# Performance work log

Measured on AMD Instinct MI355X. Metric: run time of the kernel, lower is better.

## Reference

```python
import jax, jax.numpy as jnp
import numpy as np

MAX_REL = 16  # block_size//2 = 32//2

def _rel_buckets(T):
    r = jnp.arange(T)
    rel = r[None, :] - r[:, None]              # [T,T] = j - i
    return jnp.clip(rel, -MAX_REL, MAX_REL) + MAX_REL  # [T,T] in [0, 2*MAX_REL]

def setup_inputs() -> dict:
    key = jax.random.key(0)
    ks = jax.random.split(key, 6)
    B, T, C, H = 16, 1024, 64, 64
    x = jax.random.normal(ks[0], (B, T, C), dtype=jnp.float32)
    mask = jnp.tril(jnp.ones((T, T), dtype=jnp.int32))
    Wq = jax.random.normal(ks[1], (C, H), dtype=jnp.float32) * 0.1
    Wk = jax.random.normal(ks[2], (C, H), dtype=jnp.float32) * 0.1
    Wv = jax.random.normal(ks[3], (C, H), dtype=jnp.float32) * 0.1
    rel_key_emb = jax.random.normal(ks[4], (2 * MAX_REL + 1, H), dtype=jnp.float32) * 0.1
    rel_value_emb = jax.random.normal(ks[5], (2 * MAX_REL + 1, H), dtype=jnp.float32) * 0.1
    return {"x": x, "mask": mask, "Wq": Wq, "Wk": Wk, "Wv": Wv,
            "rel_key_emb": rel_key_emb, "rel_value_emb": rel_value_emb}

def reference(x, mask, Wq, Wk, Wv, rel_key_emb, rel_value_emb):
    B, T, C = x.shape
    H = Wq.shape[1]
    scale = H ** -0.5
    q = x @ Wq  # [B,T,H]
    k = x @ Wk
    v = x @ Wv
    buckets = _rel_buckets(T)                 # [T,T] int
    rel_k = rel_key_emb[buckets]              # [T,T,H]
    rel_v = rel_value_emb[buckets]            # [T,T,H]
    content_scores = jnp.einsum('bth,bsh->bts', q, k) * scale     # [B,T,T]
    position_scores = jnp.einsum('bth,tsh->bts', q, rel_k) * scale
    scores = content_scores + position_scores
    scores = jnp.where(mask[None, :, :] == 0, -jnp.inf, scores)
    wei = jax.nn.softmax(scores, axis=-1)     # [B,T,T]  (dropout is identity in eval)
    content_out = jnp.einsum('bts,bsh->bth', wei, v)
    position_out = jnp.einsum('bts,tsh->bth', wei, rel_v)
    return (content_out + position_out, wei)
```

## Files before the change

kernel.cpp:

```cpp
#include <hip/hip_runtime.h>
#include <cstdint>
#include <cstddef>

typedef unsigned short u16;
typedef __attribute__((ext_vector_type(8))) short s16x8;
typedef __attribute__((ext_vector_type(4))) float f32x4;

#define MFMA16(a, b, c) __builtin_amdgcn_mfma_f32_16x16x32_bf16(a, b, c, 0, 0, 0)

#define B_ 16
#define T_ 1024
#define H_ 64
#define SCALE 0.125f

static __device__ __forceinline__ u16 f2bf(float f) {
    unsigned u = __float_as_uint(f);
    u += 0x7FFFu + ((u >> 16) & 1u);
    return (u16)(u >> 16);
}
static __device__ __forceinline__ float bf2f(u16 h) {
    return __uint_as_float((unsigned)h << 16);
}
static __device__ __forceinline__ s16x8 ld8(const u16* p) {
    return *(const s16x8*)p;
}
static __device__ __forceinline__ s16x8 pack8f(const float* p) {
    s16x8 r;
#pragma unroll
    for (int i = 0; i < 8; i++) r[i] = (short)f2bf(p[i]);
    return r;
}

__global__ __launch_bounds__(256) void proj_kernel(
    const float* __restrict__ x, const float* __restrict__ Wq,
    const float* __restrict__ Wk, const float* __restrict__ Wv,
    u16* __restrict__ Qb, u16* __restrict__ Kb, u16* __restrict__ VTb) {
    __shared__ u16 wtb[64][72];
    const int tid = threadIdx.x;
    const int m = blockIdx.y;
    const float* Wm = (m == 0) ? Wq : (m == 1) ? Wk : Wv;
    for (int idx = tid; idx < 1024; idx += 256) {
        const int cin = idx >> 4, c = (idx & 15) << 2;
        const float4 v = *(const float4*)(Wm + cin * 64 + c);
        wtb[c + 0][cin] = f2bf(v.x);
        wtb[c + 1][cin] = f2bf(v.y);
        wtb[c + 2][cin] = f2bf(v.z);
        wtb[c + 3][cin] = f2bf(v.w);
    }
    __syncthreads();
    const int w = tid >> 6, l = tid & 63, lg = l >> 4, lc = l & 15;
    const int base = blockIdx.x * 64 + w * 16;
    const float* xp = x + (size_t)(base + lc) * 64 + lg * 8;
    const s16x8 aX0 = pack8f(xp), aX1 = pack8f(xp + 32);
#pragma unroll
    for (int nt = 0; nt < 4; nt++) {
        const s16x8 b0 = ld8(&wtb[nt * 16 + lc][lg * 8]);
        const s16x8 b1 = ld8(&wtb[nt * 16 + lc][32 + lg * 8]);
        f32x4 acc = {0.f, 0.f, 0.f, 0.f};
        acc = MFMA16(aX0, b0, acc);
        acc = MFMA16(aX1, b1, acc);
        const int col = nt * 16 + lc;
        if (m == 2) {
            const int t0 = base + lg * 4;
            const int bb = t0 >> 10, tl = t0 & 1023;
            ushort4 pk;
            pk.x = f2bf(acc[0]); pk.y = f2bf(acc[1]);
            pk.z = f2bf(acc[2]); pk.w = f2bf(acc[3]);
            *(ushort4*)(VTb + ((size_t)(bb * 64 + col)) * 1024 + tl) = pk;
        } else {
            u16* dst = (m == 0) ? Qb : Kb;
#pragma unroll
            for (int reg = 0; reg < 4; reg++)
                dst[(size_t)(base + lg * 4 + reg) * 64 + col] = f2bf(acc[reg]);
        }
    }
}

__global__ __launch_bounds__(256) void attn_kernel(
    const u16* __restrict__ Qb, const u16* __restrict__ Kb,
    const u16* __restrict__ VTb, const float* __restrict__ rel_key_emb,
    const float* __restrict__ rel_value_emb,
    float* __restrict__ out, float* __restrict__ wei) {
    union EU {
        u16 e[16 * 1024];
        float obuf[4][16][64];
    };
    __shared__ __align__(16) EU sh;
    __shared__ __align__(16) float rv_lds[17][64];
    __shared__ float p_lds[16][33];
    __shared__ float band_lds[16][17];
    __shared__ float sum_lds[4][16];

    const int tid = threadIdx.x, w = tid >> 6, l = tid & 63, lg = l >> 4, lc = l & 15;
    const int bx = blockIdx.x;
    const int s = bx >> 8, i = bx & 255, q = i >> 4;
    const int b = i & 15;
    const int R = (s == 0) ? 63 - q : (s == 1) ? 32 + q : (s == 2) ? 31 - q : q;
    const int wrow = R << 4;
    const int ntiles = R + 1;
    char* eb = (char*)sh.e;

    for (int idx = tid; idx < 17 * 64; idx += 256)
        rv_lds[idx >> 6][idx & 63] = rel_value_emb[idx];
    for (int idx = tid; idx < 16 * 17; idx += 256)
        ((float*)band_lds)[idx] = 0.f;

    const u16* qp = Qb + (size_t)(b * 1024 + wrow + lc) * 64 + lg * 8;
    const s16x8 aQ0 = ld8(qp), aQ1 = ld8(qp + 32);

    if (w == 0) {
#pragma unroll
        for (int nt = 0; nt < 2; nt++) {
            const float* rp = rel_key_emb + (nt * 16 + lc) * 64 + lg * 8;
            const s16x8 b0 = pack8f(rp), b1 = pack8f(rp + 32);
            f32x4 acc = {0.f, 0.f, 0.f, 0.f};
            acc = MFMA16(aQ0, b0, acc);
            acc = MFMA16(aQ1, b1, acc);
#pragma unroll
            for (int reg = 0; reg < 4; reg++)
                p_lds[lg * 4 + reg][nt * 16 + lc] = acc[reg] * SCALE;
        }
    }
    __syncthreads();

    float p0r[4];
#pragma unroll
    for (int reg = 0; reg < 4; reg++) p0r[reg] = p_lds[lg * 4 + reg][0];

    const int P = (ntiles + 1) >> 1;
    const int pq = P >> 2, prem = P & 3;
    const int pstart = w * pq + (w < prem ? w : prem);
    const int pcnt = pq + (w < prem ? 1 : 0);
    const int cbeg = pstart << 1;
    const int cend0 = cbeg + (pcnt << 1);
    const int cend = cend0 < ntiles ? cend0 : ntiles;

    float sum[4] = {0.f, 0.f, 0.f, 0.f};
    f32x4 accO[4];
#pragma unroll
    for (int nt = 0; nt < 4; nt++) accO[nt] = (f32x4){0.f, 0.f, 0.f, 0.f};

    for (int j = 0; j < pcnt; j++) {
        const int sc0 = cbeg + 2 * j;
#pragma unroll
        for (int half = 0; half < 2; half++) {
            const int sc = sc0 + half;
            const int colb = (sc * 16 + lc) * 2;
            if (sc < cend) {
                const u16* kp = Kb + (size_t)(b * 1024 + sc * 16 + lc) * 64 + lg * 8;
                const s16x8 b0 = ld8(kp), b1 = ld8(kp + 32);
                f32x4 acc = {0.f, 0.f, 0.f, 0.f};
                acc = MFMA16(aQ0, b0, acc);
                acc = MFMA16(aQ1, b1, acc);
                const bool bandt = (sc >= ntiles - 2);
#pragma unroll
                for (int reg = 0; reg < 4; reg++) {
                    const int t16 = lg * 4 + reg;
                    const int d = (sc * 16 + lc) - (wrow + t16);
                    float pv = p0r[reg];
                    bool msk = false;
                    if (bandt) {
                        if (d > 0) msk = true;
                        else if (d > -16) pv = p_lds[t16][d + 16];
                    }
                    const float ev = msk ? 0.f : __expf(acc[reg] * SCALE + pv);
                    sum[reg] += ev;
                    *(u16*)(eb + t16 * 2048 + (colb ^ ((t16 & 7) << 4))) = f2bf(ev);
                    if (bandt && d > -16 && d <= 0) band_lds[t16][d + 15] = ev;
                }
            } else {
#pragma unroll
                for (int reg = 0; reg < 4; reg++) {
                    const int t16 = lg * 4 + reg;
                    *(u16*)(eb + t16 * 2048 + (colb ^ ((t16 & 7) << 4))) = 0;
                }
            }
        }
        const int pcolb = sc0 * 32;
        const s16x8 aW =
            *(const s16x8*)(eb + lc * 2048 + ((pcolb + lg * 16) ^ ((lc & 7) << 4)));
#pragma unroll
        for (int nt = 0; nt < 4; nt++) {
            const s16x8 bV =
                ld8(VTb + (size_t)(b * 64 + nt * 16 + lc) * 1024 + sc0 * 16 + lg * 8);
            accO[nt] = MFMA16(aW, bV, accO[nt]);
        }
    }
#pragma unroll
    for (int reg = 0; reg < 4; reg++) {
        sum[reg] += __shfl_xor(sum[reg], 1);
        sum[reg] += __shfl_xor(sum[reg], 2);
        sum[reg] += __shfl_xor(sum[reg], 4);
        sum[reg] += __shfl_xor(sum[reg], 8);
    }
    if (lc == 0) {
#pragma unroll
        for (int reg = 0; reg < 4; reg++) sum_lds[w][lg * 4 + reg] = sum[reg];
    }
    __syncthreads();

    float inv[4];
#pragma unroll
    for (int reg = 0; reg < 4; reg++) {
        const int r = lg * 4 + reg;
        inv[reg] =
            1.0f / (sum_lds[0][r] + sum_lds[1][r] + sum_lds[2][r] + sum_lds[3][r]);
    }
#pragma unroll
    for (int nt = 0; nt < 4; nt++)
#pragma unroll
        for (int reg = 0; reg < 4; reg++) accO[nt][reg] *= inv[reg];

    {
        const int r = tid >> 4;
        const float invr =
            1.0f / (sum_lds[0][r] + sum_lds[1][r] + sum_lds[2][r] + sum_lds[3][r]);
        const int climit = ntiles << 4;
        const int xr = (r & 7) << 4;
        float* wp = wei + ((size_t)b << 20) + (size_t)(wrow + r) * 1024;
        for (int c = (tid & 15) << 2; c < 1024; c += 64) {
            float4 v;
            if (c < climit) {
                const ushort4 ev = *(const ushort4*)(eb + r * 2048 + ((c * 2) ^ xr));
                v.x = bf2f(ev.x) * invr;
                v.y = bf2f(ev.y) * invr;
                v.z = bf2f(ev.z) * invr;
                v.w = bf2f(ev.w) * invr;
            } else {
                v = make_float4(0.f, 0.f, 0.f, 0.f);
            }
            *(float4*)(wp + c) = v;
        }
    }
    __syncthreads();

#pragma unroll
    for (int nt = 0; nt < 4; nt++)
#pragma unroll
        for (int reg = 0; reg < 4; reg++)
            sh.obuf[w][lg * 4 + reg][nt * 16 + lc] = accO[nt][reg];
    __syncthreads();

    {
        const int r = tid >> 4, h = (tid & 15) << 2;
        const float invr =
            1.0f / (sum_lds[0][r] + sum_lds[1][r] + sum_lds[2][r] + sum_lds[3][r]);
        const float4 o0 = *(const float4*)&sh.obuf[0][r][h];
        const float4 o1 = *(const float4*)&sh.obuf[1][r][h];
        const float4 o2 = *(const float4*)&sh.obuf[2][r][h];
        const float4 o3 = *(const float4*)&sh.obuf[3][r][h];
        float a0 = o0.x + o1.x + o2.x + o3.x;
        float a1 = o0.y + o1.y + o2.y + o3.y;
        float a2 = o0.z + o1.z + o2.z + o3.z;
        float a3 = o0.w + o1.w + o2.w + o3.w;
        float bsum = 0.f;
#pragma unroll
        for (int k = 0; k < 16; k++) bsum += band_lds[r][k];
        const float w0 = 1.f - invr * bsum;
        const float4 rv0 = *(const float4*)&rv_lds[0][h];
        a0 += w0 * rv0.x; a1 += w0 * rv0.y; a2 += w0 * rv0.z; a3 += w0 * rv0.w;
#pragma unroll
        for (int k = 0; k < 16; k++) {
            const float bw = band_lds[r][k] * invr;
            const float4 rvk = *(const float4*)&rv_lds[k + 1][h];
            a0 += bw * rvk.x; a1 += bw * rvk.y; a2 += bw * rvk.z; a3 += bw * rvk.w;
        }
        float4 ov; ov.x = a0; ov.y = a1; ov.z = a2; ov.w = a3;
        *(float4*)(out + (size_t)(b * 1024 + wrow + r) * 64 + h) = ov;
    }
}

extern "C" void kernel_launch(void* const* d_in, const int* in_sizes, int n_in,
                              void* d_out, int out_size, void* d_ws, size_t ws_size,
                              hipStream_t stream) {
    const float* x = (const float*)d_in[0];
    const float* Wq = (const float*)d_in[2];
    const float* Wk = (const float*)d_in[3];
    const float* Wv = (const float*)d_in[4];
    const float* rk = (const float*)d_in[5];
    const float* rvv = (const float*)d_in[6];

    float* out = (float*)d_out;
    float* wei = out + (size_t)B_ * T_ * H_;

    u16* Qb = (u16*)d_ws;
    u16* Kb = Qb + (size_t)B_ * T_ * H_;
    u16* VTb = Kb + (size_t)B_ * T_ * H_;

    proj_kernel<<<dim3(256, 3), 256, 0, stream>>>(x, Wq, Wk, Wv, Qb, Kb, VTb);
    attn_kernel<<<dim3(1024), 256, 0, stream>>>(Qb, Kb, VTb, rk, rvv, out, wei);
}
```

Measured before the change: 39.96 us.

## Split attention-weight output into separate recompute kernel using stored row normalizers

The attention kernel no longer keeps the full 16x1024 bf16 probability row block in LDS or writes the 64 MB wei matrix. It stores only per-row inverse sums, and its LDS scratch shrinks to a small per-wave 16x32 tile. A new third kernel recomputes QK^T plus the positional bias and exp, scales by the stored inverse, and writes wei with nontemporal stores. The aim is higher occupancy and more streaming-friendly writes in the attention kernel, paid for with recomputed scores and an extra launch. Recomputing in fp32 from the bf16 score rather than from the bf16-rounded exp may also shift wei values slightly.

Result: slower. 53.81 us (+34.7%).

```diff
diff --git a/kernel.cpp b/kernel.cpp
--- a/kernel.cpp
+++ b/kernel.cpp
@@ -18,9 +18,6 @@
     u += 0x7FFFu + ((u >> 16) & 1u);
     return (u16)(u >> 16);
 }
-static __device__ __forceinline__ float bf2f(u16 h) {
-    return __uint_as_float((unsigned)h << 16);
-}
 static __device__ __forceinline__ s16x8 ld8(const u16* p) {
     return *(const s16x8*)p;
 }
@@ -29,6 +26,11 @@
 #pragma unroll
     for (int i = 0; i < 8; i++) r[i] = (short)f2bf(p[i]);
     return r;
+}
+static __device__ __forceinline__ void slotmap(int bx, int& R, int& b) {
+    const int s = bx >> 8, i = bx & 255, q = i >> 4;
+    b = i & 15;
+    R = (s == 0) ? 63 - q : (s == 1) ? 32 + q : (s == 2) ? 31 - q : q;
 }
 
 __global__ __launch_bounds__(256) void proj_kernel(
@@ -80,25 +82,22 @@
     const u16* __restrict__ Qb, const u16* __restrict__ Kb,
     const u16* __restrict__ VTb, const float* __restrict__ rel_key_emb,
     const float* __restrict__ rel_value_emb,
-    float* __restrict__ out, float* __restrict__ wei) {
-    union EU {
-        u16 e[16 * 1024];
+    float* __restrict__ out, float* __restrict__ invArr) {
+    union SU {
+        u16 w_lds[4][16][40];
         float obuf[4][16][64];
     };
-    __shared__ __align__(16) EU sh;
+    __shared__ __align__(16) SU sh;
     __shared__ __align__(16) float rv_lds[17][64];
     __shared__ float p_lds[16][33];
     __shared__ float band_lds[16][17];
     __shared__ float sum_lds[4][16];
 
     const int tid = threadIdx.x, w = tid >> 6, l = tid & 63, lg = l >> 4, lc = l & 15;
-    const int bx = blockIdx.x;
-    const int s = bx >> 8, i = bx & 255, q = i >> 4;
-    const int b = i & 15;
-    const int R = (s == 0) ? 63 - q : (s == 1) ? 32 + q : (s == 2) ? 31 - q : q;
+    int R, b;
+    slotmap(blockIdx.x, R, b);
     const int wrow = R << 4;
     const int ntiles = R + 1;
-    char* eb = (char*)sh.e;
 
     for (int idx = tid; idx < 17 * 64; idx += 256)
         rv_lds[idx >> 6][idx & 63] = rel_value_emb[idx];
@@ -145,7 +144,6 @@
 #pragma unroll
         for (int half = 0; half < 2; half++) {
             const int sc = sc0 + half;
-            const int colb = (sc * 16 + lc) * 2;
             if (sc < cend) {
                 const u16* kp = Kb + (size_t)(b * 1024 + sc * 16 + lc) * 64 + lg * 8;
                 const s16x8 b0 = ld8(kp), b1 = ld8(kp + 32);
@@ -165,20 +163,16 @@
                     }
                     const float ev = msk ? 0.f : __expf(acc[reg] * SCALE + pv);
                     sum[reg] += ev;
-                    *(u16*)(eb + t16 * 2048 + (colb ^ ((t16 & 7) << 4))) = f2bf(ev);
+                    sh.w_lds[w][t16][half * 16 + lc] = f2bf(ev);
                     if (bandt && d > -16 && d <= 0) band_lds[t16][d + 15] = ev;
                 }
             } else {
 #pragma unroll
-                for (int reg = 0; reg < 4; reg++) {
-                    const int t16 = lg * 4 + reg;
-                    *(u16*)(eb + t16 * 2048 + (colb ^ ((t16 & 7) << 4))) = 0;
-                }
+                for (int reg = 0; reg < 4; reg++)
+                    sh.w_lds[w][lg * 4 + reg][half * 16 + lc] = 0;
             }
         }
-        const int pcolb = sc0 * 32;
-        const s16x8 aW =
-            *(const s16x8*)(eb + lc * 2048 + ((pcolb + lg * 16) ^ ((lc & 7) << 4)));
+        const s16x8 aW = ld8(&sh.w_lds[w][lc][lg * 8]);
 #pragma unroll
         for (int nt = 0; nt < 4; nt++) {
             const s16x8 bV =
@@ -209,42 +203,15 @@
 #pragma unroll
     for (int nt = 0; nt < 4; nt++)
 #pragma unroll
-        for (int reg = 0; reg < 4; reg++) accO[nt][reg] *= inv[reg];
-
-    {
-        const int r = tid >> 4;
-        const float invr =
-            1.0f / (sum_lds[0][r] + sum_lds[1][r] + sum_lds[2][r] + sum_lds[3][r]);
-        const int climit = ntiles << 4;
-        const int xr = (r & 7) << 4;
-        float* wp = wei + ((size_t)b << 20) + (size_t)(wrow + r) * 1024;
-        for (int c = (tid & 15) << 2; c < 1024; c += 64) {
-            float4 v;
-            if (c < climit) {
-                const ushort4 ev = *(const ushort4*)(eb + r * 2048 + ((c * 2) ^ xr));
-                v.x = bf2f(ev.x) * invr;
-                v.y = bf2f(ev.y) * invr;
-                v.z = bf2f(ev.z) * invr;
-                v.w = bf2f(ev.w) * invr;
-            } else {
-                v = make_float4(0.f, 0.f, 0.f, 0.f);
-            }
-            *(float4*)(wp + c) = v;
-        }
-    }
-    __syncthreads();
-
-#pragma unroll
-    for (int nt = 0; nt < 4; nt++)
-#pragma unroll
         for (int reg = 0; reg < 4; reg++)
-            sh.obuf[w][lg * 4 + reg][nt * 16 + lc] = accO[nt][reg];
+            sh.obuf[w][lg * 4 + reg][nt * 16 + lc] = accO[nt][reg] * inv[reg];
     __syncthreads();
 
     {
         const int r = tid >> 4, h = (tid & 15) << 2;
         const float invr =
             1.0f / (sum_lds[0][r] + sum_lds[1][r] + sum_lds[2][r] + sum_lds[3][r]);
+        if ((tid & 15) == 0) invArr[b * 1024 + wrow + r] = invr;
         const float4 o0 = *(const float4*)&sh.obuf[0][r][h];
         const float4 o1 = *(const float4*)&sh.obuf[1][r][h];
         const float4 o2 = *(const float4*)&sh.obuf[2][r][h];
@@ -270,6 +237,77 @@
     }
 }
 
+__global__ __launch_bounds__(256) void wei_kernel(
+    const u16* __restrict__ Qb, const u16* __restrict__ Kb,
+    const float* __restrict__ rel_key_emb, const float* __restrict__ invArr,
+    float* __restrict__ wei) {
+    __shared__ float p_lds[16][33];
+    const int tid = threadIdx.x, w = tid >> 6, l = tid & 63, lg = l >> 4, lc = l & 15;
+    int rt, b;
+    slotmap(blockIdx.x, rt, b);
+    const int wrow = rt << 4;
+
+    const u16* qp = Qb + (size_t)(b * 1024 + wrow + lc) * 64 + lg * 8;
+    const s16x8 bQ0 = ld8(qp), bQ1 = ld8(qp + 32);
+    const float inv_t = invArr[b * 1024 + wrow + lc];
+
+    if (w == 0) {
+#pragma unroll
+        for (int nt = 0; nt < 2; nt++) {
+            const float* rp = rel_key_emb + (nt * 16 + lc) * 64 + lg * 8;
+            const s16x8 r0 = pack8f(rp), r1 = pack8f(rp + 32);
+            f32x4 acc = {0.f, 0.f, 0.f, 0.f};
+            acc = MFMA16(bQ0, r0, acc);
+            acc = MFMA16(bQ1, r1, acc);
+#pragma unroll
+            for (int reg = 0; reg < 4; reg++)
+                p_lds[lg * 4 + reg][nt * 16 + lc] = acc[reg] * SCALE;
+        }
+    }
+    __syncthreads();
+    const float p0 = p_lds[lc][0];
+
+    s16x8 k0, k1;
+    if (w <= rt) {
+        const u16* kp = Kb + (size_t)(b * 1024 + w * 16 + lc) * 64 + lg * 8;
+        k0 = ld8(kp);
+        k1 = ld8(kp + 32);
+    }
+    const f32x4 zz = {0.f, 0.f, 0.f, 0.f};
+    for (int ct = w; ct < 64; ct += 4) {
+        float* wp =
+            wei + ((size_t)b << 20) + (size_t)(wrow + lc) * 1024 + ct * 16 + lg * 4;
+        if (ct <= rt) {
+            const s16x8 a0 = k0, a1 = k1;
+            if (ct + 4 <= rt) {
+                const u16* kp =
+                    Kb + (size_t)(b * 1024 + (ct + 4) * 16 + lc) * 64 + lg * 8;
+                k0 = ld8(kp);
+                k1 = ld8(kp + 32);
+            }
+            f32x4 acc = {0.f, 0.f, 0.f, 0.f};
+            acc = MFMA16(a0, bQ0, acc);
+            acc = MFMA16(a1, bQ1, acc);
+            const bool bandt = (ct >= rt - 1);
+            f32x4 v;
+#pragma unroll
+            for (int reg = 0; reg < 4; reg++) {
+                const int d = (ct * 16 + lg * 4 + reg) - (wrow + lc);
+                float pv = p0;
+                bool msk = false;
+                if (bandt) {
+                    if (d > 0) msk = true;
+                    else if (d > -16) pv = p_lds[lc][d + 16];
+                }
+                v[reg] = msk ? 0.f : __expf(acc[reg] * SCALE + pv) * inv_t;
+            }
+            __builtin_nontemporal_store(v, (f32x4*)wp);
+        } else {
+            __builtin_nontemporal_store(zz, (f32x4*)wp);
+        }
+    }
+}
+
 extern "C" void kernel_launch(void* const* d_in, const int* in_sizes, int n_in,
                               void* d_out, int out_size, void* d_ws, size_t ws_size,
                               hipStream_t stream) {
@@ -286,7 +324,9 @@
     u16* Qb = (u16*)d_ws;
     u16* Kb = Qb + (size_t)B_ * T_ * H_;
     u16* VTb = Kb + (size_t)B_ * T_ * H_;
+    float* invArr = (float*)(VTb + (size_t)B_ * H_ * T_);
 
     proj_kernel<<<dim3(256, 3), 256, 0, stream>>>(x, Wq, Wk, Wv, Qb, Kb, VTb);
-    attn_kernel<<<dim3(1024), 256, 0, stream>>>(Qb, Kb, VTb, rk, rvv, out, wei);
-}
+    attn_kernel<<<dim3(1024), 256, 0, stream>>>(Qb, Kb, VTb, rk, rvv, out, invArr);
+    wei_kernel<<<dim3(1024), 256, 0, stream>>>(Qb, Kb, rk, invArr, wei);
+}
```

## Split attention column pairs across eight waves per block instead of four

Applied to the files above, without the earlier changes.

Doubles the attention block to 512 threads so the key-tile pairs of each 16-row query tile are divided among eight waves rather than four. This shortens the serial per-wave loop for long causal rows. The per-wave partial sums and output buffers grow to eight slots and are reduced at the end, and the wei write loop is re-indexed for the larger block. The LDS staging of rel_value_emb is dropped in favour of direct global reads in the epilogue. The trade-off is more cross-wave reduction work, idle waves on short rows, and higher register pressure under the new launch bounds.

Result: slower. 50.87 us (+27.3%).

```diff
diff --git a/kernel.cpp b/kernel.cpp
--- a/kernel.cpp
+++ b/kernel.cpp
@@ -29,6 +29,11 @@
 #pragma unroll
     for (int i = 0; i < 8; i++) r[i] = (short)f2bf(p[i]);
     return r;
+}
+static __device__ __forceinline__ void slotmap(int bx, int& R, int& b) {
+    const int s = bx >> 8, i = bx & 255, q = i >> 4;
+    b = i & 15;
+    R = (s == 0) ? 63 - q : (s == 1) ? 32 + q : (s == 2) ? 31 - q : q;
 }
 
 __global__ __launch_bounds__(256) void proj_kernel(
@@ -76,34 +81,28 @@
     }
 }
 
-__global__ __launch_bounds__(256) void attn_kernel(
+__global__ __launch_bounds__(512, 8) void attn_kernel(
     const u16* __restrict__ Qb, const u16* __restrict__ Kb,
     const u16* __restrict__ VTb, const float* __restrict__ rel_key_emb,
     const float* __restrict__ rel_value_emb,
     float* __restrict__ out, float* __restrict__ wei) {
     union EU {
         u16 e[16 * 1024];
-        float obuf[4][16][64];
+        float obuf[8][16][64];
     };
     __shared__ __align__(16) EU sh;
-    __shared__ __align__(16) float rv_lds[17][64];
     __shared__ float p_lds[16][33];
     __shared__ float band_lds[16][17];
-    __shared__ float sum_lds[4][16];
+    __shared__ float sum_lds[8][16];
 
     const int tid = threadIdx.x, w = tid >> 6, l = tid & 63, lg = l >> 4, lc = l & 15;
-    const int bx = blockIdx.x;
-    const int s = bx >> 8, i = bx & 255, q = i >> 4;
-    const int b = i & 15;
-    const int R = (s == 0) ? 63 - q : (s == 1) ? 32 + q : (s == 2) ? 31 - q : q;
+    int R, b;
+    slotmap(blockIdx.x, R, b);
     const int wrow = R << 4;
     const int ntiles = R + 1;
     char* eb = (char*)sh.e;
 
-    for (int idx = tid; idx < 17 * 64; idx += 256)
-        rv_lds[idx >> 6][idx & 63] = rel_value_emb[idx];
-    for (int idx = tid; idx < 16 * 17; idx += 256)
-        ((float*)band_lds)[idx] = 0.f;
+    if (tid < 16 * 17) ((float*)band_lds)[tid] = 0.f;
 
     const u16* qp = Qb + (size_t)(b * 1024 + wrow + lc) * 64 + lg * 8;
     const s16x8 aQ0 = ld8(qp), aQ1 = ld8(qp + 32);
@@ -128,7 +127,7 @@
     for (int reg = 0; reg < 4; reg++) p0r[reg] = p_lds[lg * 4 + reg][0];
 
     const int P = (ntiles + 1) >> 1;
-    const int pq = P >> 2, prem = P & 3;
+    const int pq = P >> 3, prem = P & 7;
     const int pstart = w * pq + (w < prem ? w : prem);
     const int pcnt = pq + (w < prem ? 1 : 0);
     const int cbeg = pstart << 1;
@@ -140,40 +139,42 @@
 #pragma unroll
     for (int nt = 0; nt < 4; nt++) accO[nt] = (f32x4){0.f, 0.f, 0.f, 0.f};
 
+    auto scoreHalf = [&](const int sc) {
+        const int colb = (sc * 16 + lc) * 2;
+        const u16* kp = Kb + (size_t)(b * 1024 + sc * 16 + lc) * 64 + lg * 8;
+        const s16x8 b0 = ld8(kp), b1 = ld8(kp + 32);
+        f32x4 acc = {0.f, 0.f, 0.f, 0.f};
+        acc = MFMA16(aQ0, b0, acc);
+        acc = MFMA16(aQ1, b1, acc);
+        const bool bandt = (sc >= ntiles - 2);
+#pragma unroll
+        for (int reg = 0; reg < 4; reg++) {
+            const int t16 = lg * 4 + reg;
+            const int d = (sc * 16 + lc) - (wrow + t16);
+            float pv = p0r[reg];
+            bool msk = false;
+            if (bandt) {
+                if (d > 0) msk = true;
+                else if (d > -16) pv = p_lds[t16][d + 16];
+            }
+            const float ev = msk ? 0.f : __expf(acc[reg] * SCALE + pv);
+            sum[reg] += ev;
+            *(u16*)(eb + t16 * 2048 + (colb ^ ((t16 & 7) << 4))) = f2bf(ev);
+            if (bandt && d > -16 && d <= 0) band_lds[t16][d + 15] = ev;
+        }
+    };
+
     for (int j = 0; j < pcnt; j++) {
         const int sc0 = cbeg + 2 * j;
-#pragma unroll
-        for (int half = 0; half < 2; half++) {
-            const int sc = sc0 + half;
-            const int colb = (sc * 16 + lc) * 2;
-            if (sc < cend) {
-                const u16* kp = Kb + (size_t)(b * 1024 + sc * 16 + lc) * 64 + lg * 8;
-                const s16x8 b0 = ld8(kp), b1 = ld8(kp + 32);
-                f32x4 acc = {0.f, 0.f, 0.f, 0.f};
-                acc = MFMA16(aQ0, b0, acc);
-                acc = MFMA16(aQ1, b1, acc);
-                const bool bandt = (sc >= ntiles - 2);
-#pragma unroll
-                for (int reg = 0; reg < 4; reg++) {
-                    const int t16 = lg * 4 + reg;
-                    const int d = (sc * 16 + lc) - (wrow + t16);
-                    float pv = p0r[reg];
-                    bool msk = false;
-                    if (bandt) {
-                        if (d > 0) msk = true;
-                        else if (d > -16) pv = p_lds[t16][d + 16];
-                    }
-                    const float ev = msk ? 0.f : __expf(acc[reg] * SCALE + pv);
-                    sum[reg] += ev;
-                    *(u16*)(eb + t16 * 2048 + (colb ^ ((t16 & 7) << 4))) = f2bf(ev);
-                    if (bandt && d > -16 && d <= 0) band_lds[t16][d + 15] = ev;
-                }
-            } else {
-#pragma unroll
-                for (int reg = 0; reg < 4; reg++) {
-                    const int t16 = lg * 4 + reg;
-                    *(u16*)(eb + t16 * 2048 + (colb ^ ((t16 & 7) << 4))) = 0;
-                }
+        scoreHalf(sc0);
+        if (sc0 + 1 < cend) {
+            scoreHalf(sc0 + 1);
+        } else {
+            const int colb = ((sc0 + 1) * 16 + lc) * 2;
+#pragma unroll
+            for (int reg = 0; reg < 4; reg++) {
+                const int t16 = lg * 4 + reg;
+                *(u16*)(eb + t16 * 2048 + (colb ^ ((t16 & 7) << 4))) = 0;
             }
         }
         const int pcolb = sc0 * 32;
@@ -199,12 +200,22 @@
     }
     __syncthreads();
 
+    float invr_row;
+    {
+        const int r = (tid >> 5) & 15;
+        float s = 0.f;
+#pragma unroll
+        for (int k = 0; k < 8; k++) s += sum_lds[k][r];
+        invr_row = 1.0f / s;
+    }
     float inv[4];
 #pragma unroll
     for (int reg = 0; reg < 4; reg++) {
         const int r = lg * 4 + reg;
-        inv[reg] =
-            1.0f / (sum_lds[0][r] + sum_lds[1][r] + sum_lds[2][r] + sum_lds[3][r]);
+        float s = 0.f;
+#pragma unroll
+        for (int k = 0; k < 8; k++) s += sum_lds[k][r];
+        inv[reg] = 1.0f / s;
     }
 #pragma unroll
     for (int nt = 0; nt < 4; nt++)
@@ -212,20 +223,18 @@
         for (int reg = 0; reg < 4; reg++) accO[nt][reg] *= inv[reg];
 
     {
-        const int r = tid >> 4;
-        const float invr =
-            1.0f / (sum_lds[0][r] + sum_lds[1][r] + sum_lds[2][r] + sum_lds[3][r]);
+        const int r = tid >> 5;
         const int climit = ntiles << 4;
         const int xr = (r & 7) << 4;
         float* wp = wei + ((size_t)b << 20) + (size_t)(wrow + r) * 1024;
-        for (int c = (tid & 15) << 2; c < 1024; c += 64) {
+        for (int c = (tid & 31) << 2; c < 1024; c += 128) {
             float4 v;
             if (c < climit) {
                 const ushort4 ev = *(const ushort4*)(eb + r * 2048 + ((c * 2) ^ xr));
-                v.x = bf2f(ev.x) * invr;
-                v.y = bf2f(ev.y) * invr;
-                v.z = bf2f(ev.z) * invr;
-                v.w = bf2f(ev.w) * invr;
+                v.x = bf2f(ev.x) * invr_row;
+                v.y = bf2f(ev.y) * invr_row;
+                v.z = bf2f(ev.z) * invr_row;
+                v.w = bf2f(ev.w) * invr_row;
             } else {
                 v = make_float4(0.f, 0.f, 0.f, 0.f);
             }
@@ -241,28 +250,28 @@
             sh.obuf[w][lg * 4 + reg][nt * 16 + lc] = accO[nt][reg];
     __syncthreads();
 
-    {
+    if (tid < 256) {
         const int r = tid >> 4, h = (tid & 15) << 2;
-        const float invr =
-            1.0f / (sum_lds[0][r] + sum_lds[1][r] + sum_lds[2][r] + sum_lds[3][r]);
-        const float4 o0 = *(const float4*)&sh.obuf[0][r][h];
-        const float4 o1 = *(const float4*)&sh.obuf[1][r][h];
-        const float4 o2 = *(const float4*)&sh.obuf[2][r][h];
-        const float4 o3 = *(const float4*)&sh.obuf[3][r][h];
-        float a0 = o0.x + o1.x + o2.x + o3.x;
-        float a1 = o0.y + o1.y + o2.y + o3.y;
-        float a2 = o0.z + o1.z + o2.z + o3.z;
-        float a3 = o0.w + o1.w + o2.w + o3.w;
+        float srow = 0.f;
+#pragma unroll
+        for (int k = 0; k < 8; k++) srow += sum_lds[k][r];
+        const float invr = 1.0f / srow;
+        float a0 = 0.f, a1 = 0.f, a2 = 0.f, a3 = 0.f;
+#pragma unroll
+        for (int k = 0; k < 8; k++) {
+            const float4 o = *(const float4*)&sh.obuf[k][r][h];
+            a0 += o.x; a1 += o.y; a2 += o.z; a3 += o.w;
+        }
         float bsum = 0.f;
 #pragma unroll
         for (int k = 0; k < 16; k++) bsum += band_lds[r][k];
         const float w0 = 1.f - invr * bsum;
-        const float4 rv0 = *(const float4*)&rv_lds[0][h];
+        const float4 rv0 = *(const float4*)(rel_value_emb + h);
         a0 += w0 * rv0.x; a1 += w0 * rv0.y; a2 += w0 * rv0.z; a3 += w0 * rv0.w;
 #pragma unroll
         for (int k = 0; k < 16; k++) {
             const float bw = band_lds[r][k] * invr;
-            const float4 rvk = *(const float4*)&rv_lds[k + 1][h];
+            const float4 rvk = *(const float4*)(rel_value_emb + (k + 1) * 64 + h);
             a0 += bw * rvk.x; a1 += bw * rvk.y; a2 += bw * rvk.z; a3 += bw * rvk.w;
         }
         float4 ov; ov.x = a0; ov.y = a1; ov.z = a2; ov.w = a3;
@@ -288,5 +297,5 @@
     u16* VTb = Kb + (size_t)B_ * T_ * H_;
 
     proj_kernel<<<dim3(256, 3), 256, 0, stream>>>(x, Wq, Wk, Wv, Qb, Kb, VTb);
-    attn_kernel<<<dim3(1024), 256, 0, stream>>>(Qb, Kb, VTb, rk, rvv, out, wei);
-}
+    attn_kernel<<<dim3(1024), 512, 0, stream>>>(Qb, Kb, VTb, rk, rvv, out, wei);
+}
```
